# Performance work log

Hardware: AMD Instinct MI355X
Metric: run time of the kernel (lower is better)

## Reference

```python
import jax, jax.numpy as jnp
import numpy as np

EPS = 1e-5

def instance_norm(x):
    # x: [B, n, C]; InstanceNorm1d normalizes over the n (length) axis per channel, no affine
    mean = jnp.mean(x, axis=1, keepdims=True)
    var = jnp.var(x, axis=1, keepdims=True)  # biased variance, matches torch
    return (x - mean) / jnp.sqrt(var + EPS)

def gat_layer(h, w, a_src, a_dst, b):
    # h: [B, n, d_in]; w: [H, d_in, d_out]; a_src/a_dst: [H, d_out, 1]; b: [d_out]
    h_ = jnp.einsum('bnd,hdk->bhnk', h, w)               # [B, H, n, d_out]
    s_src = jnp.einsum('bhnk,hk->bhn', h_, a_src[..., 0])  # [B, H, n]
    s_dst = jnp.einsum('bhnk,hk->bhn', h_, a_dst[..., 0])  # [B, H, n]
    attn = s_src[:, :, :, None] + s_dst[:, :, None, :]    # [B, H, n, n]
    attn = jax.nn.leaky_relu(attn, negative_slope=0.2)
    attn = jax.nn.softmax(attn, axis=-1)
    return jnp.einsum('bhnm,bhmk->bhnk', attn, h_) + b    # [B, H, n, d_out]

def setup_inputs() -> dict:
    key = jax.random.key(0)
    ks = jax.random.split(key, 7)
    B, N = 4, 4096
    x = jax.random.normal(ks[0], (B, N, 64), dtype=jnp.float32)
    g = 1.414
    def xavier(k, shape):
        fan_in, fan_out = shape[-2], shape[-1]
        lim = g * np.sqrt(6.0 / (fan_in + fan_out))
        return jax.random.uniform(k, shape, jnp.float32, -lim, lim)
    return {
        'x': x,
        'w0': xavier(ks[1], (4, 64, 32)),
        'a_src0': xavier(ks[2], (4, 32, 1)),
        'a_dst0': xavier(ks[3], (4, 32, 1)),
        'b0': jnp.zeros((32,), jnp.float32),
        'w1': xavier(ks[4], (1, 128, 64)),
        'a_src1': xavier(ks[5], (1, 64, 1)),
        'a_dst1': xavier(ks[6], (1, 64, 1)),
        'b1': jnp.zeros((64,), jnp.float32),
    }

def reference(x, w0, a_src0, a_dst0, b0, w1, a_src1, a_dst1, b1):
    B, N = x.shape[:2]
    # layer 0: norm -> GAT(4 heads) -> concat heads -> ELU
    h = instance_norm(x)
    h = gat_layer(h, w0, a_src0, a_dst0, b0)              # [B, 4, N, 32]
    h = jnp.transpose(h, (0, 2, 1, 3)).reshape(B, N, -1)  # [B, N, 128]
    h = jax.nn.elu(h)
    # layer 1: norm -> GAT(1 head) -> squeeze head
    h = instance_norm(h)
    h = gat_layer(h, w1, a_src1, a_dst1, b1)              # [B, 1, N, 64]
    return h[:, 0]                                        # [B, N, 64]
```

## Files before the change

### kernel.cpp

```cpp
#include <hip/hip_runtime.h>
#include <math.h>

#define N_ 4096

static constexpr size_t OFF_HP0    = 2048;
static constexpr size_t OFF_ELU    = 2048;
static constexpr size_t OFF_SS0    = 2099200;
static constexpr size_t OFF_SD0    = 2164736;
static constexpr size_t OFF_RUNS0  = 2230272;
static constexpr size_t OFF_SV0    = 2361344;
static constexpr size_t OFF_PM0    = 2426880;
static constexpr size_t OFF_EP0    = 2492416;
static constexpr size_t OFF_EN0    = 2557952;
static constexpr size_t OFF_CPP0   = 2623488;
static constexpr size_t OFF_CPN0   = 2689040;
static constexpr size_t OFF_RAWP0  = 2754592;
static constexpr size_t OFF_RAWN0  = 2885664;
static constexpr size_t OFF_BP0    = 3016736;
static constexpr size_t OFF_BN0    = 3148320;
static constexpr size_t OFF_TPP0   = 3279904;
static constexpr size_t OFF_TPN0   = 5377568;
static constexpr size_t OFF_HP1    = 3279904;
static constexpr size_t OFF_SS1    = 4328480;
static constexpr size_t OFF_SD1    = 4344864;
static constexpr size_t OFF_RUNS1  = 4361248;
static constexpr size_t OFF_SV1    = 4394016;
static constexpr size_t OFF_PM1    = 4410400;
static constexpr size_t OFF_EP1    = 4426784;
static constexpr size_t OFF_EN1    = 4443168;
static constexpr size_t OFF_CPP1   = 4459552;
static constexpr size_t OFF_CPN1   = 4475940;
static constexpr size_t OFF_RAWP1  = 4492328;
static constexpr size_t OFF_RAWN1  = 4557864;
static constexpr size_t OFF_BP1    = 4623400;
static constexpr size_t OFF_BN1    = 4689192;
static constexpr size_t OFF_TPP1   = 4754984;
static constexpr size_t OFF_TPN1   = 5803816;
static constexpr size_t OFF_S0P    = 6852648;
static constexpr size_t OFF_S1P    = 6869032;

__device__ __forceinline__ unsigned f2s(float f){
  unsigned u=__float_as_uint(f);
  return u^((u&0x80000000u)?0xFFFFFFFFu:0x80000000u);
}
__device__ __forceinline__ float s2f(unsigned s){
  unsigned u=(s&0x80000000u)?(s^0x80000000u):~s;
  return __uint_as_float(u);
}
__device__ __forceinline__ void fma4(float4& a, float s, float4 w){
  a.x+=s*w.x; a.y+=s*w.y; a.z+=s*w.z; a.w+=s*w.w;
}
__device__ __forceinline__ float dot4(float4 a, float4 b){
  return a.x*b.x+a.y*b.y+a.z*b.z+a.w*b.w;
}

template<int C>
__global__ void kstats(const float* __restrict__ x, float* __restrict__ statsP){
  int blk=blockIdx.x; int b=blk>>5;
  int tid=threadIdx.x;
  const int RPT=256/C;
  const int IT=128/RPT;
  int c=tid%C, rl=tid/C;
  const float* xb=x+(size_t)b*N_*C;
  float s1=0.f,s2=0.f;
  int r0=(blk&31)*128+rl;
  for(int i=0;i<IT;i++){
    float v=xb[(size_t)(r0+i*RPT)*C+c];
    s1+=v;s2+=v*v;
  }
  __shared__ float sh1[256],sh2[256];
  sh1[tid]=s1;sh2[tid]=s2;__syncthreads();
  if(tid<C){
    float a1=0.f,a2=0.f;
    for(int g=0;g<RPT;g++){a1+=sh1[g*C+tid];a2+=sh2[g*C+tid];}
    statsP[((size_t)blk*C+tid)*2+0]=a1;
    statsP[((size_t)blk*C+tid)*2+1]=a2;
  }
}

__global__ void __launch_bounds__(256) kproj0(
                       const float* __restrict__ x, const float* __restrict__ statsP,
                       const float* __restrict__ w0, const float* __restrict__ asrc,
                       const float* __restrict__ adst, float* __restrict__ hp,
                       float* __restrict__ ss, float* __restrict__ sd){
  __shared__ float4 w4[512];
  __shared__ float mean[64],rstd[64];
  __shared__ float red1[256],red2[256];
  __shared__ float ssP[1024],sdP[1024];
  int tid=threadIdx.x;
  int blk=blockIdx.x;
  int b=blk>>6, h=(blk>>4)&3, nb=blk&15;
  const float4* wg=(const float4*)w0+(size_t)h*512;
  w4[tid]=wg[tid]; w4[tid+256]=wg[tid+256];
  {
    int tc=tid&63, tg=tid>>6;
    float a1=0.f,a2=0.f;
    #pragma unroll 2
    for(int g=tg*8;g<tg*8+8;g++){
      a1+=statsP[((size_t)(b*32+g)*64+tc)*2+0];
      a2+=statsP[((size_t)(b*32+g)*64+tc)*2+1];
    }
    red1[tid]=a1; red2[tid]=a2;
  }
  __syncthreads();
  if(tid<64){
    float s1=red1[tid]+red1[tid+64]+red1[tid+128]+red1[tid+192];
    float s2=red2[tid]+red2[tid+64]+red2[tid+128]+red2[tid+192];
    float mu=s1*(1.0f/N_);
    float var=s2*(1.0f/N_)-mu*mu;
    mean[tid]=mu; rstd[tid]=rsqrtf(var+1e-5f);
  }
  __syncthreads();
  int w=tid>>6, lane=tid&63;
  int n0=nb*256+lane;
  const float4* xb=(const float4*)(x+((size_t)b*N_+n0)*64);
  float4 acc[4][2];
  #pragma unroll
  for(int r=0;r<4;r++){acc[r][0]=make_float4(0,0,0,0);acc[r][1]=make_float4(0,0,0,0);}
  for(int ch=0;ch<8;ch++){
    float4 wr[8][2];
    #pragma unroll
    for(int dd=0;dd<8;dd++){
      wr[dd][0]=w4[(ch*8+dd)*8+w*2+0];
      wr[dd][1]=w4[(ch*8+dd)*8+w*2+1];
    }
    float4 mn0=*(const float4*)&mean[ch*8], mn1=*(const float4*)&mean[ch*8+4];
    float4 rs0=*(const float4*)&rstd[ch*8], rs1=*(const float4*)&rstd[ch*8+4];
    #pragma unroll
    for(int r=0;r<4;r++){
      float4 t0=xb[(size_t)r*1024+ch*2+0];
      float4 t1=xb[(size_t)r*1024+ch*2+1];
      float hv[8];
      hv[0]=(t0.x-mn0.x)*rs0.x; hv[1]=(t0.y-mn0.y)*rs0.y;
      hv[2]=(t0.z-mn0.z)*rs0.z; hv[3]=(t0.w-mn0.w)*rs0.w;
      hv[4]=(t1.x-mn1.x)*rs1.x; hv[5]=(t1.y-mn1.y)*rs1.y;
      hv[6]=(t1.z-mn1.z)*rs1.z; hv[7]=(t1.w-mn1.w)*rs1.w;
      #pragma unroll
      for(int dd=0;dd<8;dd++){
        fma4(acc[r][0],hv[dd],wr[dd][0]);
        fma4(acc[r][1],hv[dd],wr[dd][1]);
      }
    }
  }
  float4 a1v0=((const float4*)asrc)[h*8+w*2+0];
  float4 a1v1=((const float4*)asrc)[h*8+w*2+1];
  float4 a2v0=((const float4*)adst)[h*8+w*2+0];
  float4 a2v1=((const float4*)adst)[h*8+w*2+1];
  int p=b*4+h;
  #pragma unroll
  for(int r=0;r<4;r++){
    ssP[w*256+r*64+lane]=dot4(acc[r][0],a1v0)+dot4(acc[r][1],a1v1);
    sdP[w*256+r*64+lane]=dot4(acc[r][0],a2v0)+dot4(acc[r][1],a2v1);
    float4* o4=(float4*)(hp+((size_t)p*N_+n0+r*64)*32+w*8);
    o4[0]=acc[r][0]; o4[1]=acc[r][1];
  }
  __syncthreads();
  {
    float s=ssP[tid]+ssP[256+tid]+ssP[512+tid]+ssP[768+tid];
    float d=sdP[tid]+sdP[256+tid]+sdP[512+tid]+sdP[768+tid];
    ss[(size_t)p*N_+nb*256+tid]=s;
    sd[(size_t)p*N_+nb*256+tid]=d;
  }
}

__global__ void __launch_bounds__(256) kproj1(
                       const float* __restrict__ x, const float* __restrict__ statsP,
                       const float* __restrict__ w1, const float* __restrict__ asrc,
                       const float* __restrict__ adst, float* __restrict__ hp,
                       float* __restrict__ ss, float* __restrict__ sd){
  __shared__ float4 w4[512];
  __shared__ float wa[128],wd[128],mean[128],rstd[128];
  __shared__ float red1[256],red2[256];
  int tid=threadIdx.x;
  int blk=blockIdx.x;
  int b=blk>>6, cgq=(blk>>4)&3, nb=blk&15;
  {
    const float4* wg=(const float4*)w1;
    int i=tid;       int d=i>>2, c=i&3; w4[i]=wg[d*16+cgq*4+c];
    i=tid+256;       d=i>>2;     c=i&3; w4[i]=wg[d*16+cgq*4+c];
  }
  {
    int tc=tid&127, tg=tid>>7;
    float a1=0.f,a2=0.f;
    #pragma unroll 4
    for(int g=tg*16;g<tg*16+16;g++){
      a1+=statsP[((size_t)(b*32+g)*128+tc)*2+0];
      a2+=statsP[((size_t)(b*32+g)*128+tc)*2+1];
    }
    red1[tid]=a1; red2[tid]=a2;
  }
  __syncthreads();
  if(tid<128){
    float s1a=0.f,s2a=0.f;
    for(int k=0;k<64;k++){float wv=w1[tid*64+k];s1a+=wv*asrc[k];s2a+=wv*adst[k];}
    wa[tid]=s1a;wd[tid]=s2a;
    float s1=red1[tid]+red1[tid+128];
    float s2=red2[tid]+red2[tid+128];
    float mu=s1*(1.0f/N_);
    float var=s2*(1.0f/N_)-mu*mu;
    mean[tid]=mu; rstd[tid]=rsqrtf(var+1e-5f);
  }
  __syncthreads();
  int w=tid>>6, lane=tid&63;
  int cg=cgq*4+w;
  int n0=nb*256+lane;
  const float4* xb=(const float4*)(x+((size_t)b*N_+n0)*128);
  float4 acc[4];
  #pragma unroll
  for(int r=0;r<4;r++) acc[r]=make_float4(0,0,0,0);
  float s1a[4]={0.f,0.f,0.f,0.f}, s2a[4]={0.f,0.f,0.f,0.f};
  bool dosum=(cgq==0)&&(w==0);
  for(int ch=0;ch<16;ch++){
    float4 wr[8];
    #pragma unroll
    for(int dd=0;dd<8;dd++) wr[dd]=w4[(ch*8+dd)*4+w];
    float4 mn0=*(const float4*)&mean[ch*8], mn1=*(const float4*)&mean[ch*8+4];
    float4 rs0=*(const float4*)&rstd[ch*8], rs1=*(const float4*)&rstd[ch*8+4];
    float4 wa0,wa1,wd0,wd1;
    if(dosum){
      wa0=*(const float4*)&wa[ch*8]; wa1=*(const float4*)&wa[ch*8+4];
      wd0=*(const float4*)&wd[ch*8]; wd1=*(const float4*)&wd[ch*8+4];
    }
    #pragma unroll
    for(int r=0;r<4;r++){
      float4 t0=xb[(size_t)r*2048+ch*2+0];
      float4 t1=xb[(size_t)r*2048+ch*2+1];
      float hv[8];
      hv[0]=(t0.x-mn0.x)*rs0.x; hv[1]=(t0.y-mn0.y)*rs0.y;
      hv[2]=(t0.z-mn0.z)*rs0.z; hv[3]=(t0.w-mn0.w)*rs0.w;
      hv[4]=(t1.x-mn1.x)*rs1.x; hv[5]=(t1.y-mn1.y)*rs1.y;
      hv[6]=(t1.z-mn1.z)*rs1.z; hv[7]=(t1.w-mn1.w)*rs1.w;
      #pragma unroll
      for(int dd=0;dd<8;dd++) fma4(acc[r],hv[dd],wr[dd]);
      if(dosum){
        s1a[r]+=hv[0]*wa0.x+hv[1]*wa0.y+hv[2]*wa0.z+hv[3]*wa0.w
               +hv[4]*wa1.x+hv[5]*wa1.y+hv[6]*wa1.z+hv[7]*wa1.w;
        s2a[r]+=hv[0]*wd0.x+hv[1]*wd0.y+hv[2]*wd0.z+hv[3]*wd0.w
               +hv[4]*wd1.x+hv[5]*wd1.y+hv[6]*wd1.z+hv[7]*wd1.w;
      }
    }
  }
  #pragma unroll
  for(int r=0;r<4;r++){
    float4* o4=(float4*)(hp+((size_t)b*N_+n0+r*64)*64+cg*4);
    o4[0]=acc[r];
  }
  if(dosum){
    #pragma unroll
    for(int r=0;r<4;r++){
      ss[(size_t)b*N_+n0+r*64]=s1a[r];
      sd[(size_t)b*N_+n0+r*64]=s2a[r];
    }
  }
}

__global__ void __launch_bounds__(256) ksort_runs(const float* __restrict__ sdst,
                                                  unsigned long long* __restrict__ runs){
  __shared__ unsigned long long sm[1024];
  int p=blockIdx.x>>2, run=blockIdx.x&3;
  int tid=threadIdx.x;
  const float* s=sdst+(size_t)p*N_+run*1024;
  for(int l=tid;l<1024;l+=256){
    unsigned key=f2s(s[l]);
    sm[l]=((unsigned long long)key<<32)|(unsigned)(run*1024+l);
  }
  for(unsigned k=2;k<=1024u;k<<=1)
    for(unsigned j=k>>1;j>0;j>>=1){
      __syncthreads();
      for(unsigned t=tid;t<512u;t+=256u){
        unsigned i=((t&~(j-1))<<1)|(t&(j-1));
        unsigned q=i|j;
        bool up=((i&k)==0);
        unsigned long long a=sm[i],b=sm[q];
        if((a>b)==up){sm[i]=b;sm[q]=a;}
      }
    }
  __syncthreads();
  unsigned long long* rg=runs+(size_t)p*N_+run*1024;
  for(int l=tid;l<1024;l+=256) rg[l]=sm[l];
}

__global__ void __launch_bounds__(1024) kmerge(const unsigned long long* __restrict__ runs,
    float* __restrict__ sv, unsigned* __restrict__ perm,
    float* __restrict__ eP, float* __restrict__ eN){
  __shared__ unsigned long long sm[4096];
  int p=blockIdx.x>>2, cg=blockIdx.x&3;
  int tid=threadIdx.x;
  const unsigned long long* rg=runs+(size_t)p*N_;
  for(int l=tid;l<4096;l+=1024) sm[l]=rg[l];
  __syncthreads();
  unsigned long long e=sm[cg*1024+tid];
  int rank=tid;
  #pragma unroll
  for(int o=0;o<4;o++){
    if(o==cg) continue;
    const unsigned long long* base=sm+o*1024;
    int lo=0,hi=1024;
    while(lo<hi){int mid=(lo+hi)>>1; if(base[mid]<e) lo=mid+1; else hi=mid;}
    rank+=lo;
  }
  unsigned long long mk=sm[1023];
  if(sm[2047]>mk) mk=sm[2047];
  if(sm[3071]>mk) mk=sm[3071];
  if(sm[4095]>mk) mk=sm[4095];
  float m=s2f((unsigned)(mk>>32));
  float v=s2f((unsigned)(e>>32));
  size_t o=(size_t)p*N_+rank;
  sv[o]=v;
  perm[o]=(unsigned)(e&0xffffffffu);
  eP[o]=expf(v-m);
  eN[o]=expf(0.2f*(v-m));
}

__device__ __forceinline__ void counts_block(const float* __restrict__ eP,
    const float* __restrict__ eN, float* __restrict__ CPP, float* __restrict__ CPN,
    int p, float* s){
  int t=threadIdx.x;
  for(int pass=0;pass<2;pass++){
    const float* e=pass?eN:eP;
    float* C=pass?CPN:CPP;
    const float4* e4=(const float4*)(e+(size_t)p*N_);
    float4 a0=e4[t*4+0],a1=e4[t*4+1],a2=e4[t*4+2],a3=e4[t*4+3];
    float lp=a0.x+a0.y+a0.z+a0.w+a1.x+a1.y+a1.z+a1.w
            +a2.x+a2.y+a2.z+a2.w+a3.x+a3.y+a3.z+a3.w;
    if(pass) __syncthreads();
    s[t]=lp; __syncthreads();
    for(int off=1;off<256;off<<=1){
      float tv=(t>=off)?s[t-off]:0.f;
      __syncthreads();
      s[t]+=tv;
      __syncthreads();
    }
    float bp=s[t]-lp;
    size_t o=(size_t)p*4097+(size_t)t*16;
    C[o+ 0]=bp; bp+=a0.x; C[o+ 1]=bp; bp+=a0.y; C[o+ 2]=bp; bp+=a0.z; C[o+ 3]=bp; bp+=a0.w;
    C[o+ 4]=bp; bp+=a1.x; C[o+ 5]=bp; bp+=a1.y; C[o+ 6]=bp; bp+=a1.z; C[o+ 7]=bp; bp+=a1.w;
    C[o+ 8]=bp; bp+=a2.x; C[o+ 9]=bp; bp+=a2.y; C[o+10]=bp; bp+=a2.z; C[o+11]=bp; bp+=a2.w;
    C[o+12]=bp; bp+=a3.x; C[o+13]=bp; bp+=a3.y; C[o+14]=bp; bp+=a3.z; C[o+15]=bp;
    if(t==255) C[(size_t)p*4097+4096]=s[255];
  }
}

__global__ void __launch_bounds__(256) ktables0(const unsigned* __restrict__ perm,
    const float* __restrict__ eP, const float* __restrict__ eN,
    const float* __restrict__ hp, float* __restrict__ TPP, float* __restrict__ TPN,
    float* __restrict__ rawP, float* __restrict__ rawN,
    float* __restrict__ CPP, float* __restrict__ CPN){
  __shared__ float s[256];
  if(blockIdx.x<16){ counts_block(eP,eN,CPP,CPN,blockIdx.x,s); return; }
  int gw=((blockIdx.x-16)*256+threadIdx.x)>>6;
  int lane=threadIdx.x&63, half=lane>>5, ch=lane&31;
  int cglob=gw*2+half;
  int p=cglob>>8, c=cglob&255;
  float aP=0.f,aN=0.f;
  for(int q=0;q<16;q++){
    int r=c*16+q;
    size_t ro=(size_t)p*N_+r;
    float ep=eP[ro],en=eN[ro];
    unsigned pr=perm[ro];
    float hv=hp[((size_t)p*N_+pr)*32+ch];
    size_t to=((size_t)p*4097+r)*32+ch;
    TPP[to]=aP; TPN[to]=aN;
    aP+=ep*hv; aN+=en*hv;
  }
  size_t bo=((size_t)p*256+c)*32+ch;
  rawP[bo]=aP; rawN[bo]=aN;
}

__global__ void __launch_bounds__(256) ktables1(const unsigned* __restrict__ perm,
    const float* __restrict__ eP, const float* __restrict__ eN,
    const float* __restrict__ hp, float* __restrict__ TPP, float* __restrict__ TPN,
    float* __restrict__ rawP, float* __restrict__ rawN,
    float* __restrict__ CPP, float* __restrict__ CPN){
  __shared__ float s[256];
  if(blockIdx.x<4){ counts_block(eP,eN,CPP,CPN,blockIdx.x,s); return; }
  int wid=((blockIdx.x-4)*256+threadIdx.x)>>6;
  int lane=threadIdx.x&63;
  int p=wid>>8, c=wid&255;
  float aP=0.f,aN=0.f;
  for(int q=0;q<16;q++){
    int r=c*16+q;
    size_t ro=(size_t)p*N_+r;
    float ep=eP[ro],en=eN[ro];
    unsigned pr=perm[ro];
    float hv=hp[((size_t)p*N_+pr)*64+lane];
    size_t to=((size_t)p*4097+r)*64+lane;
    TPP[to]=aP; TPN[to]=aN;
    aP+=ep*hv; aN+=en*hv;
  }
  size_t bo=((size_t)p*256+c)*64+lane;
  rawP[bo]=aP; rawN[bo]=aN;
}

template<int D>
__global__ void __launch_bounds__(256) kscan(const float* __restrict__ rawP,
    const float* __restrict__ rawN, float* __restrict__ bP, float* __restrict__ bN,
    float* __restrict__ TPP, float* __restrict__ TPN){
  __shared__ float ssum[256];
  int p=blockIdx.x>>1, pass=blockIdx.x&1;
  const float* src=pass?rawN:rawP;
  float* dst=pass?bN:bP;
  float* tp=pass?TPN:TPP;
  int tid=threadIdx.x;
  constexpr int SEG=256/D;
  int ch=tid&(D-1), sg=tid/D;
  const float* s0=src+(size_t)p*256*D;
  float acc=0.f;
  for(int c=sg*D;c<sg*D+D;c++) acc+=s0[c*D+ch];
  ssum[tid]=acc; __syncthreads();
  float base=0.f, tot=0.f;
  #pragma unroll
  for(int g=0;g<SEG;g++){float v=ssum[g*D+ch]; tot+=v; if(g<sg) base+=v;}
  float r=base;
  for(int c=sg*D;c<sg*D+D;c++){
    dst[((size_t)p*257+c)*D+ch]=r;
    r+=s0[c*D+ch];
  }
  if(sg==0){
    dst[((size_t)p*257+256)*D+ch]=0.f;
    tp[((size_t)p*4097+4096)*D+ch]=tot;
  }
}

__global__ void __launch_bounds__(256) keval0(const float* __restrict__ ss,
                       const float* __restrict__ sv,
                       const float* __restrict__ bP, const float* __restrict__ bN,
                       const float* __restrict__ TPP, const float* __restrict__ TPN,
                       const float* __restrict__ CPP, const float* __restrict__ CPN,
                       const float* __restrict__ bias, float* __restrict__ out){
  int gw=(blockIdx.x*256+threadIdx.x)>>6;
  int lane=threadIdx.x&63, half=lane>>5, ch=lane&31;
  int row=gw*2+half;
  int p=row>>12, i=row&4095;
  int b=p>>2, h=p&3;
  const float* svp=sv+(size_t)p*N_;
  float ssrc=ss[(size_t)p*N_+i];
  float m=svp[4095];
  float xx=ssrc+m;
  float M=xx>0.f?xx:0.2f*xx;
  float fpos=expf(xx-M),fneg=expf(0.2f*xx-M);
  float th=-ssrc;
  float s1v=svp[ch*128+127];
  unsigned long long bal=__ballot(s1v<=th);
  int c1=half?(int)__popcll(bal>>32):(int)__popcll(bal&0xFFFFFFFFull);
  int lo;
  if(c1>=32){ lo=4096; }
  else{
    float s2v=svp[c1*128+ch*4+3];
    unsigned long long bal2=__ballot(s2v<=th);
    int c2=half?(int)__popcll(bal2>>32):(int)__popcll(bal2&0xFFFFFFFFull);
    int base=c1*128+c2*4;
    float4 qv=*((const float4*)(svp+base));
    int c3=(qv.x<=th)+(qv.y<=th)+(qv.z<=th)+(qv.w<=th);
    lo=base+c3;
  }
  int c=lo>>4;
  float relP=TPP[((size_t)p*4097+lo)*32+ch];
  float relN=TPN[((size_t)p*4097+lo)*32+ch];
  float baP=bP[((size_t)p*257+c)*32+ch];
  float baN=bN[((size_t)p*257+c)*32+ch];
  float tot=TPP[((size_t)p*4097+4096)*32+ch];
  float CPl=CPP[(size_t)p*4097+lo];
  float CNl=CPN[(size_t)p*4097+lo];
  float CT =CPP[(size_t)p*4097+4096];
  float denom=fpos*(CT-CPl)+fneg*CNl;
  float v=fpos*(tot-(baP+relP))+fneg*(baN+relN);
  float r=v/denom+bias[ch];
  r=r>0.f?r:expm1f(r);
  out[((size_t)(b*N_+i))*128+h*32+ch]=r;
}

__global__ void __launch_bounds__(256) keval1(const float* __restrict__ ss,
                       const float* __restrict__ sv,
                       const float* __restrict__ bP, const float* __restrict__ bN,
                       const float* __restrict__ TPP, const float* __restrict__ TPN,
                       const float* __restrict__ CPP, const float* __restrict__ CPN,
                       const float* __restrict__ bias, float* __restrict__ out){
  int wid=(blockIdx.x*256+threadIdx.x)>>6;
  int lane=threadIdx.x&63;
  int p=wid>>12, i=wid&4095;
  const float* svp=sv+(size_t)p*N_;
  float ssrc=ss[(size_t)p*N_+i];
  float m=svp[4095];
  float xx=ssrc+m;
  float M=xx>0.f?xx:0.2f*xx;
  float fpos=expf(xx-M),fneg=expf(0.2f*xx-M);
  float th=-ssrc;
  float s1v=svp[lane*64+63];
  int c1=(int)__popcll(__ballot(s1v<=th));
  int lo;
  if(c1>=64){ lo=4096; }
  else{
    float s2v=svp[c1*64+lane];
    lo=c1*64+(int)__popcll(__ballot(s2v<=th));
  }
  int c=lo>>4;
  float relP=TPP[((size_t)p*4097+lo)*64+lane];
  float relN=TPN[((size_t)p*4097+lo)*64+lane];
  float baP=bP[((size_t)p*257+c)*64+lane];
  float baN=bN[((size_t)p*257+c)*64+lane];
  float tot=TPP[((size_t)p*4097+4096)*64+lane];
  float CPl=CPP[(size_t)p*4097+lo];
  float CNl=CPN[(size_t)p*4097+lo];
  float CT =CPP[(size_t)p*4097+4096];
  float denom=fpos*(CT-CPl)+fneg*CNl;
  float v=fpos*(tot-(baP+relP))+fneg*(baN+relN);
  out[((size_t)p*N_+i)*64+lane]=v/denom+bias[lane];
}

extern "C" void kernel_launch(void* const* d_in, const int* in_sizes, int n_in,
                              void* d_out, int out_size, void* d_ws, size_t ws_size,
                              hipStream_t stream) {
  const float* x  =(const float*)d_in[0];
  const float* w0 =(const float*)d_in[1];
  const float* as0=(const float*)d_in[2];
  const float* ad0=(const float*)d_in[3];
  const float* b0 =(const float*)d_in[4];
  const float* w1 =(const float*)d_in[5];
  const float* as1=(const float*)d_in[6];
  const float* ad1=(const float*)d_in[7];
  const float* b1 =(const float*)d_in[8];
  float* ws=(float*)d_ws;
  float* out=(float*)d_out;

  float* s0p = ws+OFF_S0P;
  float* s1p = ws+OFF_S1P;
  float* hp0 = ws+OFF_HP0;
  float* elu = ws+OFF_ELU;
  float* ss0 = ws+OFF_SS0;  float* sd0 = ws+OFF_SD0;
  unsigned long long* runs0=(unsigned long long*)(ws+OFF_RUNS0);
  float* sv0 = ws+OFF_SV0;
  unsigned* pm0=(unsigned*)(ws+OFF_PM0);
  float* eP0 = ws+OFF_EP0;  float* eN0 = ws+OFF_EN0;
  float* cP0 = ws+OFF_CPP0; float* cN0 = ws+OFF_CPN0;
  float* rP0 = ws+OFF_RAWP0; float* rN0 = ws+OFF_RAWN0;
  float* bP0 = ws+OFF_BP0;  float* bN0 = ws+OFF_BN0;
  float* tP0 = ws+OFF_TPP0; float* tN0 = ws+OFF_TPN0;
  float* hp1 = ws+OFF_HP1;
  float* ss1 = ws+OFF_SS1;  float* sd1 = ws+OFF_SD1;
  unsigned long long* runs1=(unsigned long long*)(ws+OFF_RUNS1);
  float* sv1 = ws+OFF_SV1;
  unsigned* pm1=(unsigned*)(ws+OFF_PM1);
  float* eP1 = ws+OFF_EP1;  float* eN1 = ws+OFF_EN1;
  float* cP1 = ws+OFF_CPP1; float* cN1 = ws+OFF_CPN1;
  float* rP1 = ws+OFF_RAWP1; float* rN1 = ws+OFF_RAWN1;
  float* bP1 = ws+OFF_BP1;  float* bN1 = ws+OFF_BN1;
  float* tP1 = ws+OFF_TPP1; float* tN1 = ws+OFF_TPN1;

  kstats<64><<<128,256,0,stream>>>(x,s0p);
  kproj0<<<256,256,0,stream>>>(x,s0p,w0,as0,ad0,hp0,ss0,sd0);
  ksort_runs<<<64,256,0,stream>>>(sd0,runs0);
  kmerge<<<64,1024,0,stream>>>(runs0,sv0,pm0,eP0,eN0);
  ktables0<<<528,256,0,stream>>>(pm0,eP0,eN0,hp0,tP0,tN0,rP0,rN0,cP0,cN0);
  kscan<32><<<32,256,0,stream>>>(rP0,rN0,bP0,bN0,tP0,tN0);
  keval0<<<8192,256,0,stream>>>(ss0,sv0,bP0,bN0,tP0,tN0,cP0,cN0,b0,elu);
  kstats<128><<<128,256,0,stream>>>(elu,s1p);
  kproj1<<<256,256,0,stream>>>(elu,s1p,w1,as1,ad1,hp1,ss1,sd1);
  ksort_runs<<<16,256,0,stream>>>(sd1,runs1);
  kmerge<<<16,1024,0,stream>>>(runs1,sv1,pm1,eP1,eN1);
  ktables1<<<260,256,0,stream>>>(pm1,eP1,eN1,hp1,tP1,tN1,rP1,rN1,cP1,cN1);
  kscan<64><<<8,256,0,stream>>>(rP1,rN1,bP1,bN1,tP1,tN1);
  keval1<<<4096,256,0,stream>>>(ss1,sv1,bP1,bN1,tP1,tN1,cP1,cN1,b1,out);
}
```

Before: 214.2 us.

## Fuse sort and merge kernels; fold layer-1 norm stats into ELU eval via atomics

```diff
diff --git a/kernel.cpp b/kernel.cpp
--- a/kernel.cpp
+++ b/kernel.cpp
@@ -7,7 +7,6 @@
 static constexpr size_t OFF_ELU    = 2048;
 static constexpr size_t OFF_SS0    = 2099200;
 static constexpr size_t OFF_SD0    = 2164736;
-static constexpr size_t OFF_RUNS0  = 2230272;
 static constexpr size_t OFF_SV0    = 2361344;
 static constexpr size_t OFF_PM0    = 2426880;
 static constexpr size_t OFF_EP0    = 2492416;
@@ -23,7 +22,6 @@
 static constexpr size_t OFF_HP1    = 3279904;
 static constexpr size_t OFF_SS1    = 4328480;
 static constexpr size_t OFF_SD1    = 4344864;
-static constexpr size_t OFF_RUNS1  = 4361248;
 static constexpr size_t OFF_SV1    = 4394016;
 static constexpr size_t OFF_PM1    = 4410400;
 static constexpr size_t OFF_EP1    = 4426784;
@@ -36,8 +34,8 @@
 static constexpr size_t OFF_BN1    = 4689192;
 static constexpr size_t OFF_TPP1   = 4754984;
 static constexpr size_t OFF_TPN1   = 5803816;
-static constexpr size_t OFF_S0P    = 6852648;
-static constexpr size_t OFF_S1P    = 6869032;
+static constexpr size_t OFF_S0P    = 7475232;
+static constexpr size_t OFF_ACC1   = 7491616;
 
 __device__ __forceinline__ unsigned f2s(float f){
   unsigned u=__float_as_uint(f);
@@ -55,9 +53,11 @@
 }
 
 template<int C>
-__global__ void kstats(const float* __restrict__ x, float* __restrict__ statsP){
+__global__ void kstats(const float* __restrict__ x, float* __restrict__ statsP,
+                       float* __restrict__ acc1){
   int blk=blockIdx.x; int b=blk>>5;
   int tid=threadIdx.x;
+  if(blk==0){ ((float4*)acc1)[tid]=make_float4(0.f,0.f,0.f,0.f); }
   const int RPT=256/C;
   const int IT=128/RPT;
   int c=tid%C, rl=tid/C;
@@ -164,13 +164,12 @@
 }
 
 __global__ void __launch_bounds__(256) kproj1(
-                       const float* __restrict__ x, const float* __restrict__ statsP,
+                       const float* __restrict__ x, const float* __restrict__ acc1,
                        const float* __restrict__ w1, const float* __restrict__ asrc,
                        const float* __restrict__ adst, float* __restrict__ hp,
                        float* __restrict__ ss, float* __restrict__ sd){
   __shared__ float4 w4[512];
   __shared__ float wa[128],wd[128],mean[128],rstd[128];
-  __shared__ float red1[256],red2[256];
   int tid=threadIdx.x;
   int blk=blockIdx.x;
   int b=blk>>6, cgq=(blk>>4)&3, nb=blk&15;
@@ -179,23 +178,12 @@
     int i=tid;       int d=i>>2, c=i&3; w4[i]=wg[d*16+cgq*4+c];
     i=tid+256;       d=i>>2;     c=i&3; w4[i]=wg[d*16+cgq*4+c];
   }
-  {
-    int tc=tid&127, tg=tid>>7;
-    float a1=0.f,a2=0.f;
-    #pragma unroll 4
-    for(int g=tg*16;g<tg*16+16;g++){
-      a1+=statsP[((size_t)(b*32+g)*128+tc)*2+0];
-      a2+=statsP[((size_t)(b*32+g)*128+tc)*2+1];
-    }
-    red1[tid]=a1; red2[tid]=a2;
-  }
-  __syncthreads();
   if(tid<128){
     float s1a=0.f,s2a=0.f;
     for(int k=0;k<64;k++){float wv=w1[tid*64+k];s1a+=wv*asrc[k];s2a+=wv*adst[k];}
     wa[tid]=s1a;wd[tid]=s2a;
-    float s1=red1[tid]+red1[tid+128];
-    float s2=red2[tid]+red2[tid+128];
+    float s1=acc1[((size_t)b*128+tid)*2+0];
+    float s2=acc1[((size_t)b*128+tid)*2+1];
     float mu=s1*(1.0f/N_);
     float var=s2*(1.0f/N_)-mu*mu;
     mean[tid]=mu; rstd[tid]=rsqrtf(var+1e-5f);
@@ -254,62 +242,54 @@
   }
 }
 
-__global__ void __launch_bounds__(256) ksort_runs(const float* __restrict__ sdst,
-                                                  unsigned long long* __restrict__ runs){
-  __shared__ unsigned long long sm[1024];
-  int p=blockIdx.x>>2, run=blockIdx.x&3;
-  int tid=threadIdx.x;
-  const float* s=sdst+(size_t)p*N_+run*1024;
-  for(int l=tid;l<1024;l+=256){
+__global__ void __launch_bounds__(1024) ksortmerge(const float* __restrict__ sdst,
+    float* __restrict__ sv, unsigned* __restrict__ perm,
+    float* __restrict__ eP, float* __restrict__ eN){
+  __shared__ unsigned long long sm[4096];
+  int p=blockIdx.x, tid=threadIdx.x;
+  const float* s=sdst+(size_t)p*N_;
+  for(int l=tid;l<4096;l+=1024){
     unsigned key=f2s(s[l]);
-    sm[l]=((unsigned long long)key<<32)|(unsigned)(run*1024+l);
-  }
+    sm[l]=((unsigned long long)key<<32)|(unsigned)l;
+  }
+  int run=tid>>8; unsigned tt=(unsigned)(tid&255);
+  unsigned long long* base=sm+((size_t)run<<10);
   for(unsigned k=2;k<=1024u;k<<=1)
     for(unsigned j=k>>1;j>0;j>>=1){
       __syncthreads();
-      for(unsigned t=tid;t<512u;t+=256u){
+      for(unsigned t=tt;t<512u;t+=256u){
         unsigned i=((t&~(j-1))<<1)|(t&(j-1));
         unsigned q=i|j;
         bool up=((i&k)==0);
-        unsigned long long a=sm[i],b=sm[q];
-        if((a>b)==up){sm[i]=b;sm[q]=a;}
+        unsigned long long a=base[i],b=base[q];
+        if((a>b)==up){base[i]=b;base[q]=a;}
       }
     }
   __syncthreads();
-  unsigned long long* rg=runs+(size_t)p*N_+run*1024;
-  for(int l=tid;l<1024;l+=256) rg[l]=sm[l];
-}
-
-__global__ void __launch_bounds__(1024) kmerge(const unsigned long long* __restrict__ runs,
-    float* __restrict__ sv, unsigned* __restrict__ perm,
-    float* __restrict__ eP, float* __restrict__ eN){
-  __shared__ unsigned long long sm[4096];
-  int p=blockIdx.x>>2, cg=blockIdx.x&3;
-  int tid=threadIdx.x;
-  const unsigned long long* rg=runs+(size_t)p*N_;
-  for(int l=tid;l<4096;l+=1024) sm[l]=rg[l];
-  __syncthreads();
-  unsigned long long e=sm[cg*1024+tid];
-  int rank=tid;
+  unsigned long long mk=sm[1023];
+  if(sm[2047]>mk)mk=sm[2047];
+  if(sm[3071]>mk)mk=sm[3071];
+  if(sm[4095]>mk)mk=sm[4095];
+  float m=s2f((unsigned)(mk>>32));
   #pragma unroll
-  for(int o=0;o<4;o++){
-    if(o==cg) continue;
-    const unsigned long long* base=sm+o*1024;
-    int lo=0,hi=1024;
-    while(lo<hi){int mid=(lo+hi)>>1; if(base[mid]<e) lo=mid+1; else hi=mid;}
-    rank+=lo;
-  }
-  unsigned long long mk=sm[1023];
-  if(sm[2047]>mk) mk=sm[2047];
-  if(sm[3071]>mk) mk=sm[3071];
-  if(sm[4095]>mk) mk=sm[4095];
-  float m=s2f((unsigned)(mk>>32));
-  float v=s2f((unsigned)(e>>32));
-  size_t o=(size_t)p*N_+rank;
-  sv[o]=v;
-  perm[o]=(unsigned)(e&0xffffffffu);
-  eP[o]=expf(v-m);
-  eN[o]=expf(0.2f*(v-m));
+  for(int cg=0;cg<4;cg++){
+    unsigned long long e=sm[(cg<<10)+tid];
+    int rank=tid;
+    #pragma unroll
+    for(int o=0;o<4;o++){
+      if(o==cg) continue;
+      const unsigned long long* ob=sm+((size_t)o<<10);
+      int lo=0,hi=1024;
+      while(lo<hi){int mid=(lo+hi)>>1; if(ob[mid]<e) lo=mid+1; else hi=mid;}
+      rank+=lo;
+    }
+    float v=s2f((unsigned)(e>>32));
+    size_t o2=(size_t)p*N_+rank;
+    sv[o2]=v;
+    perm[o2]=(unsigned)(e&0xffffffffu);
+    eP[o2]=expf(v-m);
+    eN[o2]=expf(0.2f*(v-m));
+  }
 }
 
 __device__ __forceinline__ void counts_block(const float* __restrict__ eP,
@@ -427,9 +407,12 @@
                        const float* __restrict__ bP, const float* __restrict__ bN,
                        const float* __restrict__ TPP, const float* __restrict__ TPN,
                        const float* __restrict__ CPP, const float* __restrict__ CPN,
-                       const float* __restrict__ bias, float* __restrict__ out){
-  int gw=(blockIdx.x*256+threadIdx.x)>>6;
-  int lane=threadIdx.x&63, half=lane>>5, ch=lane&31;
+                       const float* __restrict__ bias, float* __restrict__ out,
+                       float* __restrict__ acc1){
+  __shared__ float sm1[256],sm2[256];
+  int tid=threadIdx.x;
+  int gw=(blockIdx.x*256+tid)>>6;
+  int lane=tid&63, half=lane>>5, ch=lane&31;
   int row=gw*2+half;
   int p=row>>12, i=row&4095;
   int b=p>>2, h=p&3;
@@ -468,6 +451,20 @@
   float r=v/denom+bias[ch];
   r=r>0.f?r:expm1f(r);
   out[((size_t)(b*N_+i))*128+h*32+ch]=r;
+  sm1[tid]=r; sm2[tid]=r*r;
+  __syncthreads();
+  if(tid<64){
+    float a=sm1[tid]+sm1[tid+64]+sm1[tid+128]+sm1[tid+192];
+    float q2=sm2[tid]+sm2[tid+64]+sm2[tid+128]+sm2[tid+192];
+    sm1[tid]=a; sm2[tid]=q2;
+  }
+  __syncthreads();
+  if(tid<32){
+    float a=sm1[tid]+sm1[tid+32];
+    float q2=sm2[tid]+sm2[tid+32];
+    atomicAdd(&acc1[((size_t)b*128+h*32+tid)*2+0],a);
+    atomicAdd(&acc1[((size_t)b*128+h*32+tid)*2+1],q2);
+  }
 }
 
 __global__ void __launch_bounds__(256) keval1(const float* __restrict__ ss,
@@ -524,11 +521,10 @@
   float* out=(float*)d_out;
 
   float* s0p = ws+OFF_S0P;
-  float* s1p = ws+OFF_S1P;
+  float* acc1= ws+OFF_ACC1;
   float* hp0 = ws+OFF_HP0;
   float* elu = ws+OFF_ELU;
   float* ss0 = ws+OFF_SS0;  float* sd0 = ws+OFF_SD0;
-  unsigned long long* runs0=(unsigned long long*)(ws+OFF_RUNS0);
   float* sv0 = ws+OFF_SV0;
   unsigned* pm0=(unsigned*)(ws+OFF_PM0);
   float* eP0 = ws+OFF_EP0;  float* eN0 = ws+OFF_EN0;
@@ -538,7 +534,6 @@
   float* tP0 = ws+OFF_TPP0; float* tN0 = ws+OFF_TPN0;
   float* hp1 = ws+OFF_HP1;
   float* ss1 = ws+OFF_SS1;  float* sd1 = ws+OFF_SD1;
-  unsigned long long* runs1=(unsigned long long*)(ws+OFF_RUNS1);
   float* sv1 = ws+OFF_SV1;
   unsigned* pm1=(unsigned*)(ws+OFF_PM1);
   float* eP1 = ws+OFF_EP1;  float* eN1 = ws+OFF_EN1;
@@ -547,17 +542,14 @@
   float* bP1 = ws+OFF_BP1;  float* bN1 = ws+OFF_BN1;
   float* tP1 = ws+OFF_TPP1; float* tN1 = ws+OFF_TPN1;
 
-  kstats<64><<<128,256,0,stream>>>(x,s0p);
+  kstats<64><<<128,256,0,stream>>>(x,s0p,acc1);
   kproj0<<<256,256,0,stream>>>(x,s0p,w0,as0,ad0,hp0,ss0,sd0);
-  ksort_runs<<<64,256,0,stream>>>(sd0,runs0);
-  kmerge<<<64,1024,0,stream>>>(runs0,sv0,pm0,eP0,eN0);
+  ksortmerge<<<16,1024,0,stream>>>(sd0,sv0,pm0,eP0,eN0);
   ktables0<<<528,256,0,stream>>>(pm0,eP0,eN0,hp0,tP0,tN0,rP0,rN0,cP0,cN0);
   kscan<32><<<32,256,0,stream>>>(rP0,rN0,bP0,bN0,tP0,tN0);
-  keval0<<<8192,256,0,stream>>>(ss0,sv0,bP0,bN0,tP0,tN0,cP0,cN0,b0,elu);
-  kstats<128><<<128,256,0,stream>>>(elu,s1p);
-  kproj1<<<256,256,0,stream>>>(elu,s1p,w1,as1,ad1,hp1,ss1,sd1);
-  ksort_runs<<<16,256,0,stream>>>(sd1,runs1);
-  kmerge<<<16,1024,0,stream>>>(runs1,sv1,pm1,eP1,eN1);
+  keval0<<<8192,256,0,stream>>>(ss0,sv0,bP0,bN0,tP0,tN0,cP0,cN0,b0,elu,acc1);
+  kproj1<<<256,256,0,stream>>>(elu,acc1,w1,as1,ad1,hp1,ss1,sd1);
+  ksortmerge<<<4,1024,0,stream>>>(sd1,sv1,pm1,eP1,eN1);
   ktables1<<<260,256,0,stream>>>(pm1,eP1,eN1,hp1,tP1,tN1,rP1,rN1,cP1,cN1);
   kscan<64><<<8,256,0,stream>>>(rP1,rN1,bP1,bN1,tP1,tN1);
   keval1<<<4096,256,0,stream>>>(ss1,sv1,bP1,bN1,tP1,tN1,cP1,cN1,b1,out);
```

Result: slower. 283.8 us (+32.5%).
